# Kernel optimization log

Hardware: AMD Instinct MI355X
Metric: run time of the kernel (lower is better)

The kernel has to match this reference:

```python
import jax, jax.numpy as jnp
import numpy as np

N_NODES = 50000
N_EDGES = 400000
N_GRAPHS = 128
IN_DIM = 768
HID = 128
N_CLASSES = 11
BN_EPS = 1e-5


def _sage_conv(x, src, dst, Wl, bl, Wr):
    # PyG SAGEConv (aggr='mean'): out = lin_l(mean_{j->i} x_j) + lin_r(x_i)
    # messages flow src -> dst; nodes with no in-edges get a zero aggregate.
    n = x.shape[0]
    deg = jax.ops.segment_sum(jnp.ones_like(dst, x.dtype), dst, num_segments=n)
    agg = jax.ops.segment_sum(x[src], dst, num_segments=n)  # [N, d] gather+scatter
    agg = agg / jnp.maximum(deg, 1.0)[:, None]
    return agg @ Wl.T + bl + x @ Wr.T


def _batch_norm(x, gamma, beta):
    # training-mode BatchNorm1d: biased batch statistics over the node axis
    m = jnp.mean(x, axis=0)
    v = jnp.var(x, axis=0)
    return (x - m) * jax.lax.rsqrt(v + BN_EPS) * gamma + beta


def setup_inputs() -> dict:
    key = jax.random.key(0)
    ks = jax.random.split(key, 16)
    x = jax.random.normal(ks[0], (N_NODES, IN_DIM), dtype=jnp.float32)
    edge_index = jax.random.randint(ks[1], (2, N_EDGES), 0, N_NODES, dtype=jnp.int32)
    batch = jnp.sort(jax.random.randint(ks[2], (N_NODES,), 0, N_GRAPHS, dtype=jnp.int32))

    def lin_w(k, out_d, in_d):
        return jax.random.normal(k, (out_d, in_d), dtype=jnp.float32) * (1.0 / np.sqrt(in_d))

    params = {
        'W1l': lin_w(ks[3], HID, IN_DIM), 'b1': jnp.zeros((HID,), jnp.float32),
        'W1r': lin_w(ks[4], HID, IN_DIM),
        'g1': jnp.ones((HID,), jnp.float32), 'be1': jnp.zeros((HID,), jnp.float32),
        'W2l': lin_w(ks[5], HID, HID), 'b2': jnp.zeros((HID,), jnp.float32),
        'W2r': lin_w(ks[6], HID, HID),
        'g2': jnp.ones((HID,), jnp.float32), 'be2': jnp.zeros((HID,), jnp.float32),
        'W3l': lin_w(ks[7], HID, HID), 'b3': jnp.zeros((HID,), jnp.float32),
        'W3r': lin_w(ks[8], HID, HID),
        'g3': jnp.ones((HID,), jnp.float32), 'be3': jnp.zeros((HID,), jnp.float32),
        'Wlin': lin_w(ks[9], N_CLASSES, HID), 'blin': jnp.zeros((N_CLASSES,), jnp.float32),
    }
    return {'x': x, 'edge_index': edge_index, 'batch': batch, **params}


def reference(x, edge_index, batch,
              W1l, b1, W1r, g1, be1,
              W2l, b2, W2r, g2, be2,
              W3l, b3, W3r, g3, be3,
              Wlin, blin):
    src, dst = edge_index[0], edge_index[1]
    h = jax.nn.relu(_batch_norm(_sage_conv(x, src, dst, W1l, b1, W1r), g1, be1))
    h = jax.nn.relu(_batch_norm(_sage_conv(h, src, dst, W2l, b2, W2r), g2, be2))
    h = _batch_norm(_sage_conv(h, src, dst, W3l, b3, W3r), g3, be3)
    # global_max_pool over graph ids
    pooled = jax.ops.segment_max(h, batch, num_segments=N_GRAPHS)  # [G, HID]
    # dropout is identity at inference
    return pooled @ Wlin.T + blin  # [G, 11]
```

## Files before the change

### kernel.cpp

```cpp
#include <hip/hip_runtime.h>

#define N_NODESC 50000
#define N_EDGESC 400000
#define N_GRAPHSC 128
#define IN_DIMC 768
#define HIDC 128
#define NCLSC 11
#define BN_EPSC 1e-5f
#define NB_AGG 8
#define NREP 64
#define SCAN_NB ((N_NODESC + 255) / 256)

typedef __bf16 bf16_t;
typedef __bf16 bf16x2 __attribute__((ext_vector_type(2)));
typedef __bf16 bf16x8 __attribute__((ext_vector_type(8)));
typedef float f32x4 __attribute__((ext_vector_type(4)));

typedef __attribute__((address_space(1))) void glb_void;
typedef __attribute__((address_space(3))) void lds_void;

__device__ __forceinline__ void cp16(const void* g, void* l) {
    __builtin_amdgcn_global_load_lds((glb_void*)g, (lds_void*)l, 16, 0, 0);
}

__device__ __forceinline__ f32x4 mfma_16x16x32_bf16(bf16x8 a, bf16x8 b, f32x4 c) {
    return __builtin_amdgcn_mfma_f32_16x16x32_bf16(a, b, c, 0, 0, 0);
}

template<int MODE, int KC>
__global__ __launch_bounds__(256) void gemm_kernel(const void* __restrict__ Av,
                                                   const bf16_t* __restrict__ Wb,
                                                   const float* __restrict__ sc,
                                                   bf16_t* __restrict__ Cl,
                                                   bf16_t* __restrict__ Cr,
                                                   int M)
{
    constexpr int NK   = KC / 32;
    constexpr int AESZ = (MODE == 0) ? 4 : 2;
    constexpr int ASZ  = 64 * 32 * AESZ;
    constexpr int BSZ  = 128 * 32 * 2;
    constexpr int AISS = (MODE == 0) ? 2 : 1;
    __shared__ __align__(16) unsigned char smem[2 * ASZ + 2 * BSZ + ((MODE == 1) ? 1024 : 16)];
    unsigned char* Asm = smem;
    unsigned char* Bsm = smem + 2 * ASZ;
    float* scS = (float*)(smem + 2 * ASZ + 2 * BSZ);

    const int t    = threadIdx.x;
    const int m0   = blockIdx.x * 64;
    const int half = blockIdx.y;
    const int wid  = t >> 6;
    const int lane = t & 63;
    const int wm   = (wid >> 1) * 32;
    const int wn   = (wid & 1) * 64;
    const int l16  = lane & 15;
    const int quad = lane >> 4;

    const char* aSrc[AISS]; int aDst[AISS];
#pragma unroll
    for (int s = 0; s < AISS; s++) {
        int L = (s * 4 + wid) * 64 + lane;
        int r, c;
        if (MODE == 0) { r = L >> 3; c = (L & 7) ^ (r & 7); }
        else           { r = L >> 2; c = (L & 3) ^ ((r >> 1) & 3); }
        int row = m0 + r; if (row > M - 1) row = M - 1;
        aSrc[s] = (const char*)Av + ((size_t)row * KC + (size_t)c * (16 / AESZ)) * AESZ;
        aDst[s] = (s * 4 + wid) * 1024;
    }
    const char* bSrc[2]; int bDst[2];
#pragma unroll
    for (int s = 0; s < 2; s++) {
        int L = (s * 4 + wid) * 64 + lane;
        int r = L >> 2;
        int c = (L & 3) ^ ((r >> 1) & 3);
        bSrc[s] = (const char*)(Wb + (size_t)(half * 128 + r) * KC + c * 8);
        bDst[s] = (s * 4 + wid) * 1024;
    }

    int aOff[2][2], bOff[4];
#pragma unroll
    for (int i = 0; i < 2; i++) {
        int ra = wm + i * 16 + l16;
        if (MODE == 0) {
            aOff[i][0] = ra * 128 + (((2 * quad)     ^ (ra & 7)) * 16);
            aOff[i][1] = ra * 128 + (((2 * quad + 1) ^ (ra & 7)) * 16);
        } else {
            aOff[i][0] = ra * 64 + ((quad ^ ((ra >> 1) & 3)) * 16);
            aOff[i][1] = 0;
        }
    }
#pragma unroll
    for (int j = 0; j < 4; j++) {
        int rb = wn + j * 16 + l16;
        bOff[j] = rb * 64 + ((quad ^ ((rb >> 1) & 3)) * 16);
    }

    if (MODE == 1) {
        scS[t] = sc[t];
        __syncthreads();
    }

#pragma unroll
    for (int s = 0; s < AISS; s++) cp16(aSrc[s], Asm + aDst[s]);
#pragma unroll
    for (int s = 0; s < 2; s++)    cp16(bSrc[s], Bsm + bDst[s]);

    f32x4 acc[2][4] = {};

    for (int it = 0; it < NK; ++it) {
        const int cur = it & 1;
        if (it + 1 < NK) {
            const int nxt = 1 - cur;
            const size_t kb = (size_t)(it + 1) * 32;
#pragma unroll
            for (int s = 0; s < AISS; s++)
                cp16(aSrc[s] + kb * AESZ, Asm + nxt * ASZ + aDst[s]);
#pragma unroll
            for (int s = 0; s < 2; s++)
                cp16(bSrc[s] + kb * 2, Bsm + nxt * BSZ + bDst[s]);
            if (MODE == 0) asm volatile("s_waitcnt vmcnt(4)" ::: "memory");
            else           asm volatile("s_waitcnt vmcnt(3)" ::: "memory");
        } else {
            asm volatile("s_waitcnt vmcnt(0)" ::: "memory");
        }
        asm volatile("s_barrier" ::: "memory");

        const unsigned char* Ab = Asm + cur * ASZ;
        const unsigned char* Bb = Bsm + cur * BSZ;
        bf16x8 af[2], bfr[4];
        if (MODE == 0) {
#pragma unroll
            for (int i = 0; i < 2; i++) {
                float4 u0 = *(const float4*)(Ab + aOff[i][0]);
                float4 u1 = *(const float4*)(Ab + aOff[i][1]);
                af[i][0] = (bf16_t)u0.x; af[i][1] = (bf16_t)u0.y;
                af[i][2] = (bf16_t)u0.z; af[i][3] = (bf16_t)u0.w;
                af[i][4] = (bf16_t)u1.x; af[i][5] = (bf16_t)u1.y;
                af[i][6] = (bf16_t)u1.z; af[i][7] = (bf16_t)u1.w;
            }
        } else {
            float4 s0 = *(const float4*)&scS[it * 32 + quad * 8];
            float4 s1 = *(const float4*)&scS[it * 32 + quad * 8 + 4];
            float4 h0 = *(const float4*)&scS[HIDC + it * 32 + quad * 8];
            float4 h1 = *(const float4*)&scS[HIDC + it * 32 + quad * 8 + 4];
            float ss[8] = {s0.x, s0.y, s0.z, s0.w, s1.x, s1.y, s1.z, s1.w};
            float hh[8] = {h0.x, h0.y, h0.z, h0.w, h1.x, h1.y, h1.z, h1.w};
#pragma unroll
            for (int i = 0; i < 2; i++) {
                bf16x8 raw = *(const bf16x8*)(Ab + aOff[i][0]);
#pragma unroll
                for (int e = 0; e < 8; e++)
                    af[i][e] = (bf16_t)fmaxf(fmaf((float)raw[e], ss[e], hh[e]), 0.0f);
            }
        }
#pragma unroll
        for (int j = 0; j < 4; j++)
            bfr[j] = *(const bf16x8*)(Bb + bOff[j]);
#pragma unroll
        for (int i = 0; i < 2; i++)
#pragma unroll
            for (int j = 0; j < 4; j++)
                acc[i][j] = mfma_16x16x32_bf16(af[i], bfr[j], acc[i][j]);

        asm volatile("s_barrier" ::: "memory");
    }

    bf16_t* C = half ? Cr : Cl;
#pragma unroll
    for (int i = 0; i < 2; i++) {
        int rowb = m0 + wm + i * 16 + quad * 4;
#pragma unroll
        for (int j = 0; j < 4; j++) {
            int colh = wn + j * 16 + l16;
#pragma unroll
            for (int rr = 0; rr < 4; rr++) {
                int row = rowb + rr;
                if (row < M) C[(size_t)row * HIDC + colh] = (bf16_t)acc[i][j][rr];
            }
        }
    }
}

__global__ void wconv_kernel(const float* __restrict__ Wl, const float* __restrict__ Wr,
                             bf16_t* __restrict__ out, int KN)
{
    int i = blockIdx.x * blockDim.x + threadIdx.x;
    if (i < KN)           out[i] = (bf16_t)Wl[i];
    else if (i < 2 * KN)  out[i] = (bf16_t)Wr[i - KN];
}

__global__ void degi_kernel(const int* __restrict__ ei, int* __restrict__ degi) {
    int e = blockIdx.x * blockDim.x + threadIdx.x;
    if (e < N_EDGESC) atomicAdd(&degi[ei[N_EDGESC + e]], 1);
}

__global__ __launch_bounds__(256) void scan1_kernel(const int* __restrict__ degi,
                                                    int* __restrict__ local,
                                                    int* __restrict__ partials)
{
    __shared__ int tmp[256];
    const int t = threadIdx.x;
    const int i = blockIdx.x * 256 + t;
    int v = (i < N_NODESC) ? degi[i] : 0;
    tmp[t] = v;
    __syncthreads();
    for (int off = 1; off < 256; off <<= 1) {
        int u = (t >= off) ? tmp[t - off] : 0;
        __syncthreads();
        tmp[t] += u;
        __syncthreads();
    }
    if (i < N_NODESC) local[i] = tmp[t] - v;
    if (t == 255) partials[blockIdx.x] = tmp[255];
}

__global__ __launch_bounds__(256) void scan2_kernel(int* __restrict__ partials)
{
    __shared__ int tmp[256];
    const int t = threadIdx.x;
    int v = (t < SCAN_NB) ? partials[t] : 0;
    tmp[t] = v;
    __syncthreads();
    for (int off = 1; off < 256; off <<= 1) {
        int u = (t >= off) ? tmp[t - off] : 0;
        __syncthreads();
        tmp[t] += u;
        __syncthreads();
    }
    if (t < SCAN_NB) partials[t] = tmp[t] - v;
}

__global__ __launch_bounds__(256) void scan3_kernel(const int* __restrict__ local,
                                                    const int* __restrict__ partials,
                                                    int* __restrict__ rowptr,
                                                    int* __restrict__ cursor)
{
    const int i = blockIdx.x * 256 + threadIdx.x;
    if (i < N_NODESC) {
        int r = local[i] + partials[blockIdx.x];
        rowptr[i] = r;
        cursor[i] = r;
    }
    if (i == 0) rowptr[N_NODESC] = N_EDGESC;
}

__global__ void fill_kernel(const int* __restrict__ ei, int* __restrict__ cursor,
                            int* __restrict__ col) {
    int e = blockIdx.x * blockDim.x + threadIdx.x;
    if (e >= N_EDGESC) return;
    int d = ei[N_EDGESC + e];
    int pos = atomicAdd(&cursor[d], 1);
    col[pos] = ei[e];
}

__global__ __launch_bounds__(128) void agg_combine_kernel(const int* __restrict__ rowptr,
                                                          const int* __restrict__ col,
                                                          const bf16_t* __restrict__ Plb,
                                                          const bf16_t* __restrict__ Prb,
                                                          const float* __restrict__ bias,
                                                          bf16_t* __restrict__ Hb,
                                                          float* __restrict__ stats, int M)
{
    const int lane = threadIdx.x & 63;
    const int wv   = threadIdx.x >> 6;
    const int c0   = lane * 2;
    const float b0 = bias[c0], b1 = bias[c0 + 1];
    float s0 = 0.f, s1 = 0.f, q0 = 0.f, q1 = 0.f;
    const int n0 = blockIdx.x * NB_AGG + wv * (NB_AGG / 2);
    for (int rr = 0; rr < NB_AGG / 2; rr++) {
        int n = n0 + rr;
        if (n >= M) break;
        int lo = rowptr[n], hi = rowptr[n + 1];
        float a0 = 0.f, a1 = 0.f;
        for (int e = lo; e < hi; e += 8) {
            int rem = hi - e;
            int idx[8];
#pragma unroll
            for (int j = 0; j < 8; j++) {
                int ee = e + j; if (ee > hi - 1) ee = hi - 1;
                idx[j] = col[ee];
            }
            bf16x2 v[8];
#pragma unroll
            for (int j = 0; j < 8; j++)
                v[j] = *(const bf16x2*)&Plb[(size_t)idx[j] * HIDC + c0];
#pragma unroll
            for (int j = 0; j < 8; j++)
                if (j < rem) { a0 += (float)v[j][0]; a1 += (float)v[j][1]; }
        }
        int d = hi - lo;
        float inv = 1.0f / (float)(d > 0 ? d : 1);
        bf16x2 pr = *(const bf16x2*)&Prb[(size_t)n * HIDC + c0];
        float pre0 = fmaf(a0, inv, b0) + (float)pr[0];
        float pre1 = fmaf(a1, inv, b1) + (float)pr[1];
        bf16x2 hv; hv[0] = (bf16_t)pre0; hv[1] = (bf16_t)pre1;
        *(bf16x2*)&Hb[(size_t)n * HIDC + c0] = hv;
        s0 += pre0; s1 += pre1; q0 += pre0 * pre0; q1 += pre1 * pre1;
    }
    const int rep = (blockIdx.x * 2 + wv) & (NREP - 1);
    atomicAdd(&stats[rep * 256 + c0], s0);
    atomicAdd(&stats[rep * 256 + c0 + 1], s1);
    atomicAdd(&stats[rep * 256 + HIDC + c0], q0);
    atomicAdd(&stats[rep * 256 + HIDC + c0 + 1], q1);
}

__global__ __launch_bounds__(128) void finalize_kernel(const float* __restrict__ stats,
                                                       const float* __restrict__ g,
                                                       const float* __restrict__ be,
                                                       float* __restrict__ sc, int M)
{
    int c = threadIdx.x;
    float sum = 0.f, sumsq = 0.f;
    for (int r = 0; r < NREP; r++) {
        sum   += stats[r * 256 + c];
        sumsq += stats[r * 256 + HIDC + c];
    }
    float invM = 1.0f / (float)M;
    float mean = sum * invM;
    float var  = sumsq * invM - mean * mean;
    float s = rsqrtf(var + BN_EPSC) * g[c];
    sc[c] = s;
    sc[HIDC + c] = be[c] - mean * s;
}

__global__ __launch_bounds__(128) void pool_kernel(const bf16_t* __restrict__ Hb,
                                                   const float* __restrict__ sc,
                                                   const int* __restrict__ batch,
                                                   float* __restrict__ pooled, int M)
{
    int gph = blockIdx.x;
    int c   = threadIdx.x;
    float s = sc[c], h = sc[HIDC + c];
    int lo = 0, hi = M;
    while (lo < hi) { int m = (lo + hi) >> 1; if (batch[m] < gph) lo = m + 1; else hi = m; }
    int lo2 = lo, hi2 = M;
    while (lo2 < hi2) { int m = (lo2 + hi2) >> 1; if (batch[m] < gph + 1) lo2 = m + 1; else hi2 = m; }
    float mx = -INFINITY;
    for (int rr = lo; rr < lo2; rr++)
        mx = fmaxf(mx, fmaf((float)Hb[(size_t)rr * HIDC + c], s, h));
    pooled[gph * HIDC + c] = mx;
}

__global__ __launch_bounds__(128) void final_kernel(const float* __restrict__ pooled,
                                                    const float* __restrict__ W,
                                                    const float* __restrict__ bl,
                                                    float* __restrict__ out)
{
    __shared__ float sp[HIDC];
    int gph = blockIdx.x;
    int t   = threadIdx.x;
    sp[t] = pooled[gph * HIDC + t];
    __syncthreads();
    if (t < NCLSC) {
        float acc = bl[t];
        for (int c = 0; c < HIDC; c++) acc += sp[c] * W[t * HIDC + c];
        out[gph * NCLSC + t] = acc;
    }
}

extern "C" void kernel_launch(void* const* d_in, const int* in_sizes, int n_in,
                              void* d_out, int out_size, void* d_ws, size_t ws_size,
                              hipStream_t stream)
{
    const float* x     = (const float*)d_in[0];
    const int*   ei    = (const int*)d_in[1];
    const int*   batch = (const int*)d_in[2];
    const float* W1l = (const float*)d_in[3];
    const float* b1  = (const float*)d_in[4];
    const float* W1r = (const float*)d_in[5];
    const float* g1  = (const float*)d_in[6];
    const float* be1 = (const float*)d_in[7];
    const float* W2l = (const float*)d_in[8];
    const float* b2  = (const float*)d_in[9];
    const float* W2r = (const float*)d_in[10];
    const float* g2  = (const float*)d_in[11];
    const float* be2 = (const float*)d_in[12];
    const float* W3l = (const float*)d_in[13];
    const float* b3  = (const float*)d_in[14];
    const float* W3r = (const float*)d_in[15];
    const float* g3  = (const float*)d_in[16];
    const float* be3 = (const float*)d_in[17];
    const float* Wlin = (const float*)d_in[18];
    const float* blin = (const float*)d_in[19];

    const int M = N_NODESC;

    char* w = (char*)d_ws;
    bf16_t* Plb  = (bf16_t*)w;  w += (size_t)M * HIDC * 2;
    bf16_t* Prb  = (bf16_t*)w;  w += (size_t)M * HIDC * 2;
    bf16_t* Hb   = (bf16_t*)w;  w += (size_t)M * HIDC * 2;
    bf16_t* Wb1  = (bf16_t*)w;  w += (size_t)256 * IN_DIMC * 2;
    bf16_t* Wb2  = (bf16_t*)w;  w += (size_t)256 * HIDC * 2;
    bf16_t* Wb3  = (bf16_t*)w;  w += (size_t)256 * HIDC * 2;
    int*   rowptr= (int*)w;     w += (size_t)(M + 16) * 4;
    int*   col   = (int*)w;     w += (size_t)N_EDGESC * 4;
    int*   cursor= (int*)w;     w += (size_t)M * 4;
    int*   degi  = (int*)w;     w += (size_t)M * 4;
    int*   slocal= (int*)w;     w += (size_t)M * 4;
    int*   spart = (int*)w;     w += 256 * 4;
    float* stats = (float*)w;   w += (size_t)NREP * 256 * 4;
    float* sc    = (float*)w;   w += 256 * 4;
    float* pooled= (float*)w;   w += (size_t)N_GRAPHSC * HIDC * 4;

    const dim3 gemm_grid((M + 63) / 64, 2);
    const int agg_blocks = (M + NB_AGG - 1) / NB_AGG;
    const size_t stats_bytes = (size_t)NREP * 256 * 4;

    wconv_kernel<<<(2 * 128 * IN_DIMC + 255) / 256, 256, 0, stream>>>(W1l, W1r, Wb1, 128 * IN_DIMC);
    wconv_kernel<<<(2 * 128 * HIDC + 255) / 256, 256, 0, stream>>>(W2l, W2r, Wb2, 128 * HIDC);
    wconv_kernel<<<(2 * 128 * HIDC + 255) / 256, 256, 0, stream>>>(W3l, W3r, Wb3, 128 * HIDC);

    hipMemsetAsync(degi, 0, (size_t)M * 4, stream);
    degi_kernel<<<(N_EDGESC + 255) / 256, 256, 0, stream>>>(ei, degi);
    scan1_kernel<<<SCAN_NB, 256, 0, stream>>>(degi, slocal, spart);
    scan2_kernel<<<1, 256, 0, stream>>>(spart);
    scan3_kernel<<<SCAN_NB, 256, 0, stream>>>(slocal, spart, rowptr, cursor);
    fill_kernel<<<(N_EDGESC + 255) / 256, 256, 0, stream>>>(ei, cursor, col);

    gemm_kernel<0, IN_DIMC><<<gemm_grid, 256, 0, stream>>>(x, Wb1, nullptr, Plb, Prb, M);
    hipMemsetAsync(stats, 0, stats_bytes, stream);
    agg_combine_kernel<<<agg_blocks, 128, 0, stream>>>(rowptr, col, Plb, Prb, b1, Hb, stats, M);
    finalize_kernel<<<1, 128, 0, stream>>>(stats, g1, be1, sc, M);

    gemm_kernel<1, HIDC><<<gemm_grid, 256, 0, stream>>>(Hb, Wb2, sc, Plb, Prb, M);
    hipMemsetAsync(stats, 0, stats_bytes, stream);
    agg_combine_kernel<<<agg_blocks, 128, 0, stream>>>(rowptr, col, Plb, Prb, b2, Hb, stats, M);
    finalize_kernel<<<1, 128, 0, stream>>>(stats, g2, be2, sc, M);

    gemm_kernel<1, HIDC><<<gemm_grid, 256, 0, stream>>>(Hb, Wb3, sc, Plb, Prb, M);
    hipMemsetAsync(stats, 0, stats_bytes, stream);
    agg_combine_kernel<<<agg_blocks, 128, 0, stream>>>(rowptr, col, Plb, Prb, b3, Hb, stats, M);
    finalize_kernel<<<1, 128, 0, stream>>>(stats, g3, be3, sc, M);

    pool_kernel<<<N_GRAPHSC, 128, 0, stream>>>(Hb, sc, batch, pooled, M);
    final_kernel<<<N_GRAPHSC, 128, 0, stream>>>(pooled, Wlin, blin, (float*)d_out);
}
```

Baseline: 590.5 us.

## Enlarge GEMM tiles with triple buffering and fuse init, finalize and pool launches

The GEMM tile grows to 128 rows per block with 4x4 MFMA accumulators per wave. The A operand is triple-buffered and prefetched two steps ahead, and the wait counts are adjusted to match. The weight conversions and all memsets are folded into one init kernel. BatchNorm finalize moves into the tail of the last aggregation block via a done counter, and pooling is fused with the classifier head. The aim is to cut launch overhead and improve GEMM data reuse, at the cost of more LDS and registers per block, fewer GEMM blocks, and a serial last-block finalize.

```diff
diff --git a/kernel.cpp b/kernel.cpp
--- a/kernel.cpp
+++ b/kernel.cpp
@@ -36,21 +36,23 @@
                                                    int M)
 {
     constexpr int NK   = KC / 32;
-    constexpr int AESZ = (MODE == 0) ? 4 : 2;
-    constexpr int ASZ  = 64 * 32 * AESZ;
-    constexpr int BSZ  = 128 * 32 * 2;
-    constexpr int AISS = (MODE == 0) ? 2 : 1;
-    __shared__ __align__(16) unsigned char smem[2 * ASZ + 2 * BSZ + ((MODE == 1) ? 1024 : 16)];
+    constexpr int ASZ  = (MODE == 0) ? 16384 : 8192;
+    constexpr int BSZ  = 8192;
+    constexpr int NBB  = (MODE == 0) ? 2 : 3;
+    constexpr int AISS = (MODE == 0) ? 4 : 2;
+    constexpr int AKB  = (MODE == 0) ? 128 : 64;
+    constexpr int SCSZ = (MODE == 1) ? 1024 : 0;
+    __shared__ __align__(16) unsigned char smem[3 * ASZ + NBB * BSZ + SCSZ];
     unsigned char* Asm = smem;
-    unsigned char* Bsm = smem + 2 * ASZ;
-    float* scS = (float*)(smem + 2 * ASZ + 2 * BSZ);
+    unsigned char* Bsm = smem + 3 * ASZ;
+    float* scS = (float*)(smem + 3 * ASZ + NBB * BSZ);
 
     const int t    = threadIdx.x;
-    const int m0   = blockIdx.x * 64;
+    const int m0   = blockIdx.x * 128;
     const int half = blockIdx.y;
     const int wid  = t >> 6;
     const int lane = t & 63;
-    const int wm   = (wid >> 1) * 32;
+    const int wm   = (wid >> 1) * 64;
     const int wn   = (wid & 1) * 64;
     const int l16  = lane & 15;
     const int quad = lane >> 4;
@@ -63,7 +65,8 @@
         if (MODE == 0) { r = L >> 3; c = (L & 7) ^ (r & 7); }
         else           { r = L >> 2; c = (L & 3) ^ ((r >> 1) & 3); }
         int row = m0 + r; if (row > M - 1) row = M - 1;
-        aSrc[s] = (const char*)Av + ((size_t)row * KC + (size_t)c * (16 / AESZ)) * AESZ;
+        if (MODE == 0) aSrc[s] = (const char*)Av + ((size_t)row * KC + (size_t)c * 4) * 4;
+        else           aSrc[s] = (const char*)Av + ((size_t)row * KC + (size_t)c * 8) * 2;
         aDst[s] = (s * 4 + wid) * 1024;
     }
     const char* bSrc[2]; int bDst[2];
@@ -76,9 +79,9 @@
         bDst[s] = (s * 4 + wid) * 1024;
     }
 
-    int aOff[2][2], bOff[4];
-#pragma unroll
-    for (int i = 0; i < 2; i++) {
+    int aOff[4][2], bOff[4];
+#pragma unroll
+    for (int i = 0; i < 4; i++) {
         int ra = wm + i * 16 + l16;
         if (MODE == 0) {
             aOff[i][0] = ra * 128 + (((2 * quad)     ^ (ra & 7)) * 16);
@@ -87,11 +90,8 @@
             aOff[i][0] = ra * 64 + ((quad ^ ((ra >> 1) & 3)) * 16);
             aOff[i][1] = 0;
         }
-    }
-#pragma unroll
-    for (int j = 0; j < 4; j++) {
-        int rb = wn + j * 16 + l16;
-        bOff[j] = rb * 64 + ((quad ^ ((rb >> 1) & 3)) * 16);
+        int rb = wn + i * 16 + l16;
+        bOff[i] = rb * 64 + ((quad ^ ((rb >> 1) & 3)) * 16);
     }
 
     if (MODE == 1) {
@@ -103,33 +103,57 @@
     for (int s = 0; s < AISS; s++) cp16(aSrc[s], Asm + aDst[s]);
 #pragma unroll
     for (int s = 0; s < 2; s++)    cp16(bSrc[s], Bsm + bDst[s]);
-
-    f32x4 acc[2][4] = {};
+#pragma unroll
+    for (int s = 0; s < AISS; s++) cp16(aSrc[s] + AKB, Asm + ASZ + aDst[s]);
+    if (MODE == 1) {
+#pragma unroll
+        for (int s = 0; s < 2; s++) cp16(bSrc[s] + 64, Bsm + BSZ + bDst[s]);
+    }
+
+    f32x4 acc[4][4] = {};
 
     for (int it = 0; it < NK; ++it) {
-        const int cur = it & 1;
-        if (it + 1 < NK) {
-            const int nxt = 1 - cur;
-            const size_t kb = (size_t)(it + 1) * 32;
-#pragma unroll
-            for (int s = 0; s < AISS; s++)
-                cp16(aSrc[s] + kb * AESZ, Asm + nxt * ASZ + aDst[s]);
-#pragma unroll
-            for (int s = 0; s < 2; s++)
-                cp16(bSrc[s] + kb * 2, Bsm + nxt * BSZ + bDst[s]);
-            if (MODE == 0) asm volatile("s_waitcnt vmcnt(4)" ::: "memory");
-            else           asm volatile("s_waitcnt vmcnt(3)" ::: "memory");
+        if (it + 2 < NK) {
+            if constexpr (MODE == 0) {
+                const size_t kb1 = (size_t)(it + 1) * 64;
+                const int bb = (it + 1) & 1;
+#pragma unroll
+                for (int s = 0; s < 2; s++) cp16(bSrc[s] + kb1, Bsm + bb * BSZ + bDst[s]);
+                const size_t ka2 = (size_t)(it + 2) * 128;
+                const int ab = (it + 2) % 3;
+#pragma unroll
+                for (int s = 0; s < 4; s++) cp16(aSrc[s] + ka2, Asm + ab * ASZ + aDst[s]);
+                asm volatile("s_waitcnt vmcnt(10)" ::: "memory");
+            } else {
+                const size_t kb2 = (size_t)(it + 2) * 64;
+                const int nb = (it + 2) % 3;
+#pragma unroll
+                for (int s = 0; s < 2; s++) cp16(aSrc[s] + kb2, Asm + nb * ASZ + aDst[s]);
+#pragma unroll
+                for (int s = 0; s < 2; s++) cp16(bSrc[s] + kb2, Bsm + nb * BSZ + bDst[s]);
+                asm volatile("s_waitcnt vmcnt(8)" ::: "memory");
+            }
+        } else if (it + 1 < NK) {
+            if constexpr (MODE == 0) {
+                const size_t kb1 = (size_t)(it + 1) * 64;
+                const int bb = (it + 1) & 1;
+#pragma unroll
+                for (int s = 0; s < 2; s++) cp16(bSrc[s] + kb1, Bsm + bb * BSZ + bDst[s]);
+                asm volatile("s_waitcnt vmcnt(6)" ::: "memory");
+            } else {
+                asm volatile("s_waitcnt vmcnt(4)" ::: "memory");
+            }
         } else {
             asm volatile("s_waitcnt vmcnt(0)" ::: "memory");
         }
         asm volatile("s_barrier" ::: "memory");
 
-        const unsigned char* Ab = Asm + cur * ASZ;
-        const unsigned char* Bb = Bsm + cur * BSZ;
-        bf16x8 af[2], bfr[4];
-        if (MODE == 0) {
-#pragma unroll
-            for (int i = 0; i < 2; i++) {
+        const unsigned char* Ab = Asm + (it % 3) * ASZ;
+        const unsigned char* Bb = Bsm + ((MODE == 0) ? (it & 1) : (it % 3)) * BSZ;
+        bf16x8 af[4], bfr[4];
+        if constexpr (MODE == 0) {
+#pragma unroll
+            for (int i = 0; i < 4; i++) {
                 float4 u0 = *(const float4*)(Ab + aOff[i][0]);
                 float4 u1 = *(const float4*)(Ab + aOff[i][1]);
                 af[i][0] = (bf16_t)u0.x; af[i][1] = (bf16_t)u0.y;
@@ -145,7 +169,7 @@
             float ss[8] = {s0.x, s0.y, s0.z, s0.w, s1.x, s1.y, s1.z, s1.w};
             float hh[8] = {h0.x, h0.y, h0.z, h0.w, h1.x, h1.y, h1.z, h1.w};
 #pragma unroll
-            for (int i = 0; i < 2; i++) {
+            for (int i = 0; i < 4; i++) {
                 bf16x8 raw = *(const bf16x8*)(Ab + aOff[i][0]);
 #pragma unroll
                 for (int e = 0; e < 8; e++)
@@ -156,7 +180,7 @@
         for (int j = 0; j < 4; j++)
             bfr[j] = *(const bf16x8*)(Bb + bOff[j]);
 #pragma unroll
-        for (int i = 0; i < 2; i++)
+        for (int i = 0; i < 4; i++)
 #pragma unroll
             for (int j = 0; j < 4; j++)
                 acc[i][j] = mfma_16x16x32_bf16(af[i], bfr[j], acc[i][j]);
@@ -166,7 +190,7 @@
 
     bf16_t* C = half ? Cr : Cl;
 #pragma unroll
-    for (int i = 0; i < 2; i++) {
+    for (int i = 0; i < 4; i++) {
         int rowb = m0 + wm + i * 16 + quad * 4;
 #pragma unroll
         for (int j = 0; j < 4; j++) {
@@ -180,12 +204,29 @@
     }
 }
 
-__global__ void wconv_kernel(const float* __restrict__ Wl, const float* __restrict__ Wr,
-                             bf16_t* __restrict__ out, int KN)
-{
-    int i = blockIdx.x * blockDim.x + threadIdx.x;
-    if (i < KN)           out[i] = (bf16_t)Wl[i];
-    else if (i < 2 * KN)  out[i] = (bf16_t)Wr[i - KN];
+__global__ void init_kernel(const float* __restrict__ W1l, const float* __restrict__ W1r,
+                            const float* __restrict__ W2l, const float* __restrict__ W2r,
+                            const float* __restrict__ W3l, const float* __restrict__ W3r,
+                            bf16_t* __restrict__ Wb1, bf16_t* __restrict__ Wb2,
+                            bf16_t* __restrict__ Wb3,
+                            int* __restrict__ degi, float* __restrict__ stats,
+                            int* __restrict__ done)
+{
+    const int NW1 = 128 * IN_DIMC;
+    const int NW2 = 128 * HIDC;
+    const int NS  = 3 * NREP * 256;
+    int j = blockIdx.x * blockDim.x + threadIdx.x;
+    if (j < 2 * NW1) { Wb1[j] = (bf16_t)((j < NW1) ? W1l[j] : W1r[j - NW1]); return; }
+    j -= 2 * NW1;
+    if (j < 2 * NW2) { Wb2[j] = (bf16_t)((j < NW2) ? W2l[j] : W2r[j - NW2]); return; }
+    j -= 2 * NW2;
+    if (j < 2 * NW2) { Wb3[j] = (bf16_t)((j < NW2) ? W3l[j] : W3r[j - NW2]); return; }
+    j -= 2 * NW2;
+    if (j < NS) { stats[j] = 0.0f; return; }
+    j -= NS;
+    if (j < N_NODESC) { degi[j] = 0; return; }
+    j -= N_NODESC;
+    if (j < 16) done[j] = 0;
 }
 
 __global__ void degi_kernel(const int* __restrict__ ei, int* __restrict__ degi) {
@@ -258,12 +299,16 @@
                                                           const bf16_t* __restrict__ Prb,
                                                           const float* __restrict__ bias,
                                                           bf16_t* __restrict__ Hb,
-                                                          float* __restrict__ stats, int M)
+                                                          float* __restrict__ stats,
+                                                          const float* __restrict__ g,
+                                                          const float* __restrict__ be,
+                                                          float* __restrict__ sc,
+                                                          int* __restrict__ done, int M)
 {
     const int lane = threadIdx.x & 63;
     const int wv   = threadIdx.x >> 6;
     const int c0   = lane * 2;
-    const float b0 = bias[c0], b1 = bias[c0 + 1];
+    const float b0 = bias[c0], b1v = bias[c0 + 1];
     float s0 = 0.f, s1 = 0.f, q0 = 0.f, q1 = 0.f;
     const int n0 = blockIdx.x * NB_AGG + wv * (NB_AGG / 2);
     for (int rr = 0; rr < NB_AGG / 2; rr++) {
@@ -291,7 +336,7 @@
         float inv = 1.0f / (float)(d > 0 ? d : 1);
         bf16x2 pr = *(const bf16x2*)&Prb[(size_t)n * HIDC + c0];
         float pre0 = fmaf(a0, inv, b0) + (float)pr[0];
-        float pre1 = fmaf(a1, inv, b1) + (float)pr[1];
+        float pre1 = fmaf(a1, inv, b1v) + (float)pr[1];
         bf16x2 hv; hv[0] = (bf16_t)pre0; hv[1] = (bf16_t)pre1;
         *(bf16x2*)&Hb[(size_t)n * HIDC + c0] = hv;
         s0 += pre0; s1 += pre1; q0 += pre0 * pre0; q1 += pre1 * pre1;
@@ -301,32 +346,37 @@
     atomicAdd(&stats[rep * 256 + c0 + 1], s1);
     atomicAdd(&stats[rep * 256 + HIDC + c0], q0);
     atomicAdd(&stats[rep * 256 + HIDC + c0 + 1], q1);
-}
-
-__global__ __launch_bounds__(128) void finalize_kernel(const float* __restrict__ stats,
-                                                       const float* __restrict__ g,
-                                                       const float* __restrict__ be,
-                                                       float* __restrict__ sc, int M)
-{
-    int c = threadIdx.x;
-    float sum = 0.f, sumsq = 0.f;
-    for (int r = 0; r < NREP; r++) {
-        sum   += stats[r * 256 + c];
-        sumsq += stats[r * 256 + HIDC + c];
-    }
-    float invM = 1.0f / (float)M;
-    float mean = sum * invM;
-    float var  = sumsq * invM - mean * mean;
-    float s = rsqrtf(var + BN_EPSC) * g[c];
-    sc[c] = s;
-    sc[HIDC + c] = be[c] - mean * s;
-}
-
-__global__ __launch_bounds__(128) void pool_kernel(const bf16_t* __restrict__ Hb,
-                                                   const float* __restrict__ sc,
-                                                   const int* __restrict__ batch,
-                                                   float* __restrict__ pooled, int M)
-{
+
+    __threadfence();
+    __syncthreads();
+    __shared__ int lastv;
+    if (threadIdx.x == 0) lastv = atomicAdd(done, 1);
+    __syncthreads();
+    if (lastv == (int)gridDim.x - 1) {
+        __threadfence();
+        int c = threadIdx.x;
+        float sum = 0.f, sumsq = 0.f;
+        for (int r = 0; r < NREP; r++) {
+            sum   += __hip_atomic_load(&stats[r * 256 + c], __ATOMIC_RELAXED, __HIP_MEMORY_SCOPE_AGENT);
+            sumsq += __hip_atomic_load(&stats[r * 256 + HIDC + c], __ATOMIC_RELAXED, __HIP_MEMORY_SCOPE_AGENT);
+        }
+        float invM = 1.0f / (float)M;
+        float mean = sum * invM;
+        float var  = sumsq * invM - mean * mean;
+        float s = rsqrtf(var + BN_EPSC) * g[c];
+        sc[c] = s;
+        sc[HIDC + c] = be[c] - mean * s;
+    }
+}
+
+__global__ __launch_bounds__(128) void poolhead_kernel(const bf16_t* __restrict__ Hb,
+                                                       const float* __restrict__ sc,
+                                                       const int* __restrict__ batch,
+                                                       const float* __restrict__ Wlin,
+                                                       const float* __restrict__ blin,
+                                                       float* __restrict__ out, int M)
+{
+    __shared__ float sp[HIDC];
     int gph = blockIdx.x;
     int c   = threadIdx.x;
     float s = sc[c], h = sc[HIDC + c];
@@ -337,23 +387,12 @@
     float mx = -INFINITY;
     for (int rr = lo; rr < lo2; rr++)
         mx = fmaxf(mx, fmaf((float)Hb[(size_t)rr * HIDC + c], s, h));
-    pooled[gph * HIDC + c] = mx;
-}
-
-__global__ __launch_bounds__(128) void final_kernel(const float* __restrict__ pooled,
-                                                    const float* __restrict__ W,
-                                                    const float* __restrict__ bl,
-                                                    float* __restrict__ out)
-{
-    __shared__ float sp[HIDC];
-    int gph = blockIdx.x;
-    int t   = threadIdx.x;
-    sp[t] = pooled[gph * HIDC + t];
+    sp[c] = mx;
     __syncthreads();
-    if (t < NCLSC) {
-        float acc = bl[t];
-        for (int c = 0; c < HIDC; c++) acc += sp[c] * W[t * HIDC + c];
-        out[gph * NCLSC + t] = acc;
+    if (c < NCLSC) {
+        float acc = blin[c];
+        for (int k = 0; k < HIDC; k++) acc += sp[k] * Wlin[c * HIDC + k];
+        out[gph * NCLSC + c] = acc;
     }
 }
 
@@ -397,19 +436,21 @@
     int*   degi  = (int*)w;     w += (size_t)M * 4;
     int*   slocal= (int*)w;     w += (size_t)M * 4;
     int*   spart = (int*)w;     w += 256 * 4;
-    float* stats = (float*)w;   w += (size_t)NREP * 256 * 4;
-    float* sc    = (float*)w;   w += 256 * 4;
-    float* pooled= (float*)w;   w += (size_t)N_GRAPHSC * HIDC * 4;
-
-    const dim3 gemm_grid((M + 63) / 64, 2);
+    float* stats = (float*)w;   w += (size_t)3 * NREP * 256 * 4;
+    float* sc    = (float*)w;   w += 3 * 256 * 4;
+    int*   done  = (int*)w;     w += 16 * 4;
+
+    float* stats1 = stats;
+    float* stats2 = stats + NREP * 256;
+    float* stats3 = stats + 2 * NREP * 256;
+    float* sc1 = sc, *sc2 = sc + 256, *sc3 = sc + 512;
+
+    const dim3 gemm_grid((M + 127) / 128, 2);
     const int agg_blocks = (M + NB_AGG - 1) / NB_AGG;
-    const size_t stats_bytes = (size_t)NREP * 256 * 4;
-
-    wconv_kernel<<<(2 * 128 * IN_DIMC + 255) / 256, 256, 0, stream>>>(W1l, W1r, Wb1, 128 * IN_DIMC);
-    wconv_kernel<<<(2 * 128 * HIDC + 255) / 256, 256, 0, stream>>>(W2l, W2r, Wb2, 128 * HIDC);
-    wconv_kernel<<<(2 * 128 * HIDC + 255) / 256, 256, 0, stream>>>(W3l, W3r, Wb3, 128 * HIDC);
-
-    hipMemsetAsync(degi, 0, (size_t)M * 4, stream);
+    const int init_total = 2 * 128 * IN_DIMC + 4 * 128 * HIDC + 3 * NREP * 256 + M + 16;
+
+    init_kernel<<<(init_total + 255) / 256, 256, 0, stream>>>(W1l, W1r, W2l, W2r, W3l, W3r,
+                                                              Wb1, Wb2, Wb3, degi, stats, done);
     degi_kernel<<<(N_EDGESC + 255) / 256, 256, 0, stream>>>(ei, degi);
     scan1_kernel<<<SCAN_NB, 256, 0, stream>>>(degi, slocal, spart);
     scan2_kernel<<<1, 256, 0, stream>>>(spart);
@@ -417,20 +458,13 @@
     fill_kernel<<<(N_EDGESC + 255) / 256, 256, 0, stream>>>(ei, cursor, col);
 
     gemm_kernel<0, IN_DIMC><<<gemm_grid, 256, 0, stream>>>(x, Wb1, nullptr, Plb, Prb, M);
-    hipMemsetAsync(stats, 0, stats_bytes, stream);
-    agg_combine_kernel<<<agg_blocks, 128, 0, stream>>>(rowptr, col, Plb, Prb, b1, Hb, stats, M);
-    finalize_kernel<<<1, 128, 0, stream>>>(stats, g1, be1, sc, M);
-
-    gemm_kernel<1, HIDC><<<gemm_grid, 256, 0, stream>>>(Hb, Wb2, sc, Plb, Prb, M);
-    hipMemsetAsync(stats, 0, stats_bytes, stream);
-    agg_combine_kernel<<<agg_blocks, 128, 0, stream>>>(rowptr, col, Plb, Prb, b2, Hb, stats, M);
-    finalize_kernel<<<1, 128, 0, stream>>>(stats, g2, be2, sc, M);
-
-    gemm_kernel<1, HIDC><<<gemm_grid, 256, 0, stream>>>(Hb, Wb3, sc, Plb, Prb, M);
-    hipMemsetAsync(stats, 0, stats_bytes, stream);
-    agg_combine_kernel<<<agg_blocks, 128, 0, stream>>>(rowptr, col, Plb, Prb, b3, Hb, stats, M);
-    finalize_kernel<<<1, 128, 0, stream>>>(stats, g3, be3, sc, M);
-
-    pool_kernel<<<N_GRAPHSC, 128, 0, stream>>>(Hb, sc, batch, pooled, M);
-    final_kernel<<<N_GRAPHSC, 128, 0, stream>>>(pooled, Wlin, blin, (float*)d_out);
-}
+    agg_combine_kernel<<<agg_blocks, 128, 0, stream>>>(rowptr, col, Plb, Prb, b1, Hb,
+                                                       stats1, g1, be1, sc1, done + 0, M);
+    gemm_kernel<1, HIDC><<<gemm_grid, 256, 0, stream>>>(Hb, Wb2, sc1, Plb, Prb, M);
+    agg_combine_kernel<<<agg_blocks, 128, 0, stream>>>(rowptr, col, Plb, Prb, b2, Hb,
+                                                       stats2, g2, be2, sc2, done + 1, M);
+    gemm_kernel<1, HIDC><<<gemm_grid, 256, 0, stream>>>(Hb, Wb3, sc2, Plb, Prb, M);
+    agg_combine_kernel<<<agg_blocks, 128, 0, stream>>>(rowptr, col, Plb, Prb, b3, Hb,
+                                                       stats3, g3, be3, sc3, done + 2, M);
+    poolhead_kernel<<<N_GRAPHSC, 128, 0, stream>>>(Hb, sc3, batch, Wlin, blin, (float*)d_out, M);
+}
```

Measured after the change: 1.334 ms. 2.26x slower.
